# Optimization experiments

Hardware: AMD Instinct MI355X
Metric: run time of the kernel (lower is better)

The kernel has to match this reference:

```python
import jax, jax.numpy as jnp
import numpy as np

B, S, N_EMBD = 4, 4096, 1024
HIDDEN = 4 * N_EMBD
M_BITS_FC = 3
M_BITS_PROJ = 3
BLOCK_K = 32


def block_quant(v, m_bits, bk):
    """Block-floating-point quantization along the last (K) dim.
    Each block of `bk` elements shares an exponent derived from its max-abs;
    mantissas are rounded to `m_bits` bits. Straight-through estimator for grads."""
    *lead, K = v.shape
    vb = v.reshape(*lead, K // bk, bk)
    amax = jnp.max(jnp.abs(vb), axis=-1, keepdims=True)
    tiny = jnp.asarray(2.0 ** -126, v.dtype)
    e = jnp.floor(jnp.log2(jnp.maximum(amax, tiny)))  # shared block exponent
    scale = jnp.exp2(e - m_bits)                       # quantization step
    q = jnp.round(vb / scale) * scale
    q = vb + jax.lax.stop_gradient(q - vb)             # STE
    return q.reshape(v.shape)


def lowprec_linear(x, w, b, m_bits, bk):
    # w: [out, in]; quantize both operands along the contraction dim.
    xq = block_quant(x, m_bits, bk)
    wq = block_quant(w, m_bits, bk)
    return jnp.einsum('bsk,nk->bsn', xq, wq) + b


def setup_inputs() -> dict:
    key = jax.random.key(0)
    k0, k1, k2 = jax.random.split(key, 3)
    x = jax.random.normal(k0, (B, S, N_EMBD), jnp.float32)
    w_fc = jax.random.normal(k1, (HIDDEN, N_EMBD), jnp.float32) * (1.0 / np.sqrt(N_EMBD))
    b_fc = jnp.zeros((HIDDEN,), jnp.float32)
    w_proj = jax.random.normal(k2, (N_EMBD, HIDDEN), jnp.float32) * (1.0 / np.sqrt(HIDDEN))
    b_proj = jnp.zeros((N_EMBD,), jnp.float32)
    return {"x": x, "w_fc": w_fc, "b_fc": b_fc, "w_proj": w_proj, "b_proj": b_proj}


def reference(x, w_fc, b_fc, w_proj, b_proj):
    h = lowprec_linear(x, w_fc, b_fc, M_BITS_FC, BLOCK_K)
    h = jax.nn.gelu(h, approximate=False)  # nn.GELU default = exact erf
    return lowprec_linear(h, w_proj, b_proj, M_BITS_PROJ, BLOCK_K)
```

## Files before the change

kernel.cpp:

```cpp
#include <hip/hip_runtime.h>
#include <hip/hip_bf16.h>

using bf16 = __hip_bfloat16;
typedef __attribute__((ext_vector_type(8))) short short8;
typedef __attribute__((ext_vector_type(4))) float f32x4;

#define DI __device__ __forceinline__

constexpr int MROWS = 16384;
constexpr int EMB   = 1024;
constexpr int HID   = 4096;

DI void gload16(const bf16* g, bf16* l) {
  __builtin_amdgcn_global_load_lds((const __attribute__((address_space(1))) void*)g,
                                   (__attribute__((address_space(3))) void*)l,
                                   16, 0, 0);
}

DI void qparams(float amax, float& scale, float& inv) {
  int eb = (int)((__float_as_uint(amax) >> 23) & 255u);
  eb = eb < 4 ? 4 : eb;
  scale = __uint_as_float((unsigned)(eb - 3) << 23);
  inv   = __uint_as_float((unsigned)(257 - eb) << 23);
}

__global__ void quant32(const float* __restrict__ in, bf16* __restrict__ out, int nblk) {
  int b = blockIdx.x * blockDim.x + threadIdx.x;
  if (b >= nblk) return;
  const f32x4* p = (const f32x4*)(in + (size_t)b * 32);
  f32x4 v[8];
  float amax = 0.f;
#pragma unroll
  for (int i = 0; i < 8; i++) {
    v[i] = p[i];
    amax = fmaxf(amax, fmaxf(fmaxf(fabsf(v[i][0]), fabsf(v[i][1])),
                             fmaxf(fabsf(v[i][2]), fabsf(v[i][3]))));
  }
  float scale, inv;
  qparams(amax, scale, inv);
  alignas(16) unsigned short us[32];
#pragma unroll
  for (int i = 0; i < 8; i++)
#pragma unroll
    for (int j = 0; j < 4; j++)
      us[i * 4 + j] = (unsigned short)(__float_as_uint(rintf(v[i][j] * inv) * scale) >> 16);
  short8* o = (short8*)(out + (size_t)b * 32);
#pragma unroll
  for (int i = 0; i < 4; i++) o[i] = *(short8*)(us + i * 8);
}

#define MFMA16(a, b, c) __builtin_amdgcn_mfma_f32_16x16x32_bf16(a, b, c, 0, 0, 0)
#define SBAR()    __builtin_amdgcn_s_barrier()
#define WAITVM(n) asm volatile("s_waitcnt vmcnt(" #n ")" ::: "memory")

#define DPPMAX(x, ctrl) \
  x = fmaxf(x, __int_as_float(__builtin_amdgcn_update_dpp( \
          0, __float_as_int(x), ctrl, 0xf, 0xf, false)));
DI float redmax16(float x) {
  DPPMAX(x, 0xB1) DPPMAX(x, 0x4E) DPPMAX(x, 0x124) DPPMAX(x, 0x128)
  return x;
}

#define Q_MFMA(MB, NB, BG) \
  __builtin_amdgcn_s_setprio(1); \
  _Pragma("unroll") for (int kk = 0; kk < 2; kk++) \
  _Pragma("unroll") for (int mi = 0; mi < 4; mi++) \
  _Pragma("unroll") for (int ni = 0; ni < 2; ni++) \
    acc[(MB) + mi][(NB) + ni] = MFMA16(af[mi * 2 + kk], BG[ni * 2 + kk], acc[(MB) + mi][(NB) + ni]); \
  __builtin_amdgcn_s_setprio(0);

#define RD_AF(mh) \
  _Pragma("unroll") for (int mi = 0; mi < 4; mi++) { \
    af[mi * 2]     = ldA(db, mh, mi, 0); \
    af[mi * 2 + 1] = ldA(db, mh, mi, 1); }

#define RD_B(half, dst) \
  _Pragma("unroll") for (int ni = 0; ni < 2; ni++) { \
    dst[ni * 2]     = ldB(db, half, ni, 0); \
    dst[ni * 2 + 1] = ldB(db, half, ni, 1); }

template<int Kd, int Nd, bool GQ>
__global__ void __launch_bounds__(512, 2)
gemm8(const bf16* __restrict__ Ap, const bf16* __restrict__ Bp,
      const float* __restrict__ bias, void* __restrict__ Cout) {
  __shared__ alignas(16) bf16 SH[65536];
  bf16* Abuf = SH;
  bf16* Bbuf = SH + 32768;

  const int tid  = threadIdx.x;
  const int lane = tid & 63, wave = tid >> 6;
  const int l16  = lane & 15, lhi = lane >> 4;
  const int wr   = wave >> 2, wc  = wave & 3;

  const int idx  = blockIdx.x >> 3;
  const int xid  = blockIdx.x & 7;
  const int brow = (xid * 8 + (idx & 7)) * 256;
  const int bcol = (idx >> 3) * 256;

  const int r0 = tid >> 3;
  const int sl = (tid & 7) ^ (r0 & 7);
  const bf16* asrc = Ap + (size_t)(brow + r0) * Kd + sl * 8;
  const bf16* bsrc = Bp + (size_t)(bcol + r0) * Kd + sl * 8;

  auto stA = [&](int tt, int half) {
    const bf16* s = asrc + (size_t)half * 128 * Kd + tt * 64;
    bf16* d = Abuf + ((tt & 1) * 2 + half) * 8192 + tid * 8;
    gload16(s, d); gload16(s + (size_t)64 * Kd, d + 4096);
  };
  auto stB = [&](int tt, int half) {
    const bf16* s = bsrc + (size_t)half * 128 * Kd + tt * 64;
    bf16* d = Bbuf + ((tt & 1) * 2 + half) * 8192 + tid * 8;
    gload16(s, d); gload16(s + (size_t)64 * Kd, d + 4096);
  };

  const int sx = l16 & 7;
  const int arow = wr * 16 + l16;
  auto ldA = [&](int db, int mh, int mi, int kk) -> short8 {
    return *(const short8*)(Abuf + (db * 2 + mh) * 8192 +
                            (mi * 32 + arow) * 64 + ((kk * 4 + lhi) ^ sx) * 8);
  };
  const int brl = wc * 32 + l16;
  auto ldB = [&](int db, int half, int ni, int kk) -> short8 {
    return *(const short8*)(Bbuf + (db * 2 + half) * 8192 +
                            (brl + ni * 16) * 64 + ((kk * 4 + lhi) ^ sx) * 8);
  };

  f32x4 acc[8][4] = {};
  short8 af[8], bgl[4], bgh[4];

  constexpr int NT = Kd / 64;

  stA(0, 0); stB(0, 0); stB(0, 1); stA(0, 1);
  stA(1, 0); stB(1, 0); stB(1, 1);
  WAITVM(6); SBAR();

  for (int t = 0; t <= NT - 3; ++t) {
    const int db = t & 1;
    RD_AF(0) RD_B(0, bgl) RD_B(1, bgh)
    stA(t + 1, 1);
    Q_MFMA(0, 0, bgl)
    stA(t + 2, 0);
    Q_MFMA(0, 2, bgh)
    stB(t + 2, 0);
    RD_AF(1)
    stB(t + 2, 1);
    Q_MFMA(4, 0, bgl)
    Q_MFMA(4, 2, bgh)
    WAITVM(6); SBAR();
  }

  {
    const int db = (NT - 2) & 1;
    RD_AF(0) RD_B(0, bgl) RD_B(1, bgh)
    stA(NT - 1, 1);
    Q_MFMA(0, 0, bgl)
    Q_MFMA(0, 2, bgh)
    RD_AF(1)
    Q_MFMA(4, 0, bgl)
    Q_MFMA(4, 2, bgh)
    WAITVM(0); SBAR();
  }

  {
    const int db = (NT - 1) & 1;
    RD_AF(0) RD_B(0, bgl) RD_B(1, bgh)
    Q_MFMA(0, 0, bgl)
    Q_MFMA(0, 2, bgh)
    RD_AF(1)
    Q_MFMA(4, 0, bgl)
    Q_MFMA(4, 2, bgh)
  }

  const int cb = bcol + wc * 32;
  float bv[4];
#pragma unroll
  for (int n = 0; n < 4; n++) bv[n] = bias[cb + (n >> 1) * 128 + (n & 1) * 16 + l16];

  if constexpr (GQ) {
    bf16* outp = (bf16*)Cout;
#pragma unroll
    for (int mh2 = 0; mh2 < 2; mh2++) {
      __syncthreads();
#pragma unroll
      for (int mm = 0; mm < 4; mm++) {
        const int m = mh2 * 4 + mm;
        const int rl0 = mm * 32 + wr * 16 + lhi * 4;
#pragma unroll
        for (int r = 0; r < 4; r++) {
          float g[4];
#pragma unroll
          for (int n = 0; n < 4; n++) {
            float v = acc[m][n][r] + bv[n];
            g[n] = 0.5f * v * (1.0f + erff(v * 0.70710678118654752f));
          }
          const int rowb = (rl0 + r) * 256;
#pragma unroll
          for (int p = 0; p < 2; p++) {
            float am = redmax16(fmaxf(fabsf(g[p * 2]), fabsf(g[p * 2 + 1])));
            float sc, iv; qparams(am, sc, iv);
            const int c0 = wc * 32 + p * 128;
            SH[rowb + ((c0 + l16)      ^ (lhi << 4))] = __float2bfloat16(rintf(g[p * 2]     * iv) * sc);
            SH[rowb + ((c0 + 16 + l16) ^ (lhi << 4))] = __float2bfloat16(rintf(g[p * 2 + 1] * iv) * sc);
          }
        }
      }
      __syncthreads();
#pragma unroll
      for (int i = 0; i < 8; i++) {
        const int c   = i * 512 + tid;
        const int row = c >> 5, cc = c & 31;
        const int scc = cc ^ (((row >> 2) & 3) << 1);
        *(short8*)(outp + (size_t)(brow + mh2 * 128 + row) * Nd + bcol + cc * 8) =
            *(const short8*)(SH + (size_t)row * 256 + scc * 8);
      }
    }
  } else {
    float* outp = (float*)Cout;
#pragma unroll
    for (int m = 0; m < 8; m++) {
      const size_t rbase = (size_t)(brow + m * 32 + wr * 16 + lhi * 4);
#pragma unroll
      for (int r = 0; r < 4; r++) {
        const size_t ro = (rbase + r) * Nd;
#pragma unroll
        for (int n = 0; n < 4; n++)
          __builtin_nontemporal_store(acc[m][n][r] + bv[n],
              &outp[ro + cb + (n >> 1) * 128 + (n & 1) * 16 + l16]);
      }
    }
  }
}

extern "C" void kernel_launch(void* const* d_in, const int* in_sizes, int n_in,
                              void* d_out, int out_size, void* d_ws, size_t ws_size,
                              hipStream_t stream) {
  const float* x      = (const float*)d_in[0];
  const float* w_fc   = (const float*)d_in[1];
  const float* b_fc   = (const float*)d_in[2];
  const float* w_proj = (const float*)d_in[3];
  const float* b_proj = (const float*)d_in[4];

  char* ws = (char*)d_ws;
  bf16* xq  = (bf16*)ws;  ws += (size_t)MROWS * EMB * 2;
  bf16* wfq = (bf16*)ws;  ws += (size_t)HID * EMB * 2;
  bf16* wpq = (bf16*)ws;  ws += (size_t)EMB * HID * 2;
  bf16* hq  = (bf16*)ws;

  quant32<<<(MROWS * EMB / 32 + 255) / 256, 256, 0, stream>>>(x, xq, MROWS * EMB / 32);
  quant32<<<(HID * EMB / 32 + 255) / 256, 256, 0, stream>>>(w_fc, wfq, HID * EMB / 32);
  quant32<<<(EMB * HID / 32 + 255) / 256, 256, 0, stream>>>(w_proj, wpq, EMB * HID / 32);

  gemm8<EMB, HID, true ><<<(MROWS / 256) * (HID / 256), 512, 0, stream>>>(xq, wfq, b_fc, hq);
  gemm8<HID, EMB, false><<<(MROWS / 256) * (EMB / 256), 512, 0, stream>>>(hq, wpq, b_proj, (float*)d_out);
}
```

Before: 335.4 us.

## Give each FC GEMM block two output tiles and overlap next prefetch with epilogue

The first GEMM now launches 512 blocks, each computing two 256x256 tiles separated by 8192 rows. The prologue loads for the second tile are issued before the last MFMA stage and GELU epilogue of the first tile, which hides the pipeline fill. The epilogue also drops its LDS staging with two syncthreads and writes bf16 results straight to global memory with non-temporal scalar stores. This trades coalesced 16-byte stores for fewer barriers and frees LDS for the overlapped prefetch, at the cost of narrower, less coalesced writes.

```diff
diff --git a/kernel.cpp b/kernel.cpp
--- a/kernel.cpp
+++ b/kernel.cpp
@@ -79,7 +79,7 @@
     dst[ni * 2]     = ldB(db, half, ni, 0); \
     dst[ni * 2 + 1] = ldB(db, half, ni, 1); }
 
-template<int Kd, int Nd, bool GQ>
+template<int Kd, int Nd, bool GQ, int OT>
 __global__ void __launch_bounds__(512, 2)
 gemm8(const bf16* __restrict__ Ap, const bf16* __restrict__ Bp,
       const float* __restrict__ bias, void* __restrict__ Cout) {
@@ -92,10 +92,10 @@
   const int l16  = lane & 15, lhi = lane >> 4;
   const int wr   = wave >> 2, wc  = wave & 3;
 
-  const int idx  = blockIdx.x >> 3;
-  const int xid  = blockIdx.x & 7;
-  const int brow = (xid * 8 + (idx & 7)) * 256;
-  const int bcol = (idx >> 3) * 256;
+  int brow, bcol;
+  const int idx = blockIdx.x >> 3, xid = blockIdx.x & 7;
+  if constexpr (OT == 2) { brow = (xid * 4 + (idx & 3)) * 256; bcol = (idx >> 2) * 256; }
+  else                   { brow = (xid * 8 + (idx & 7)) * 256; bcol = (idx >> 3) * 256; }
 
   const int r0 = tid >> 3;
   const int sl = (tid & 7) ^ (r0 & 7);
@@ -130,11 +130,39 @@
 
   constexpr int NT = Kd / 64;
 
-  stA(0, 0); stB(0, 0); stB(0, 1); stA(0, 1);
-  stA(1, 0); stB(1, 0); stB(1, 1);
-  WAITVM(6); SBAR();
-
-  for (int t = 0; t <= NT - 3; ++t) {
+  const int cb = bcol + wc * 32;
+  float bv[4];
+#pragma unroll
+  for (int n = 0; n < 4; n++) bv[n] = bias[cb + (n >> 1) * 128 + (n & 1) * 16 + l16];
+
+  auto epiGQ = [&](int browseg) {
+    unsigned short* outp = (unsigned short*)Cout;
+#pragma unroll
+    for (int m = 0; m < 8; m++) {
+#pragma unroll
+      for (int r = 0; r < 4; r++) {
+        float g[4];
+#pragma unroll
+        for (int n = 0; n < 4; n++) {
+          float v = acc[m][n][r] + bv[n];
+          g[n] = 0.5f * v * (1.0f + erff(v * 0.70710678118654752f));
+        }
+        const size_t ro = (size_t)(browseg + m * 32 + wr * 16 + lhi * 4 + r) * Nd;
+#pragma unroll
+        for (int p = 0; p < 2; p++) {
+          float am = redmax16(fmaxf(fabsf(g[p * 2]), fabsf(g[p * 2 + 1])));
+          float sc, iv; qparams(am, sc, iv);
+          unsigned short* o = outp + ro + cb + p * 128 + l16;
+          __builtin_nontemporal_store(
+              (unsigned short)(__float_as_uint(rintf(g[p * 2] * iv) * sc) >> 16), o);
+          __builtin_nontemporal_store(
+              (unsigned short)(__float_as_uint(rintf(g[p * 2 + 1] * iv) * sc) >> 16), o + 16);
+        }
+      }
+    }
+  };
+
+  auto main_iter = [&](int t) {
     const int db = t & 1;
     RD_AF(0) RD_B(0, bgl) RD_B(1, bgh)
     stA(t + 1, 1);
@@ -147,7 +175,13 @@
     Q_MFMA(4, 0, bgl)
     Q_MFMA(4, 2, bgh)
     WAITVM(6); SBAR();
-  }
+  };
+
+  stA(0, 0); stB(0, 0); stB(0, 1); stA(0, 1);
+  stA(1, 0); stB(1, 0); stB(1, 1);
+  WAITVM(6); SBAR();
+
+  for (int t = 0; t <= NT - 3; ++t) main_iter(t);
 
   {
     const int db = (NT - 2) & 1;
@@ -161,71 +195,74 @@
     WAITVM(0); SBAR();
   }
 
-  {
-    const int db = (NT - 1) & 1;
-    RD_AF(0) RD_B(0, bgl) RD_B(1, bgh)
-    Q_MFMA(0, 0, bgl)
-    Q_MFMA(0, 2, bgh)
-    RD_AF(1)
-    Q_MFMA(4, 0, bgl)
-    Q_MFMA(4, 2, bgh)
-  }
-
-  const int cb = bcol + wc * 32;
-  float bv[4];
-#pragma unroll
-  for (int n = 0; n < 4; n++) bv[n] = bias[cb + (n >> 1) * 128 + (n & 1) * 16 + l16];
-
-  if constexpr (GQ) {
-    bf16* outp = (bf16*)Cout;
-#pragma unroll
-    for (int mh2 = 0; mh2 < 2; mh2++) {
-      __syncthreads();
-#pragma unroll
-      for (int mm = 0; mm < 4; mm++) {
-        const int m = mh2 * 4 + mm;
-        const int rl0 = mm * 32 + wr * 16 + lhi * 4;
+  if constexpr (OT == 2) {
+    asrc += (size_t)8192 * Kd;
+    {
+      const int db = (NT - 1) & 1;
+      stA(0, 0); stB(0, 0); stB(0, 1); stA(0, 1);
+      RD_AF(0) RD_B(0, bgl) RD_B(1, bgh)
+      Q_MFMA(0, 0, bgl)
+      Q_MFMA(0, 2, bgh)
+      RD_AF(1)
+      Q_MFMA(4, 0, bgl)
+      Q_MFMA(4, 2, bgh)
+      SBAR();
+    }
+    epiGQ(brow);
+    stA(1, 0); stB(1, 0); stB(1, 1);
+    WAITVM(6); SBAR();
+#pragma unroll
+    for (int m = 0; m < 8; m++)
+#pragma unroll
+      for (int n = 0; n < 4; n++) acc[m][n] = f32x4{0.f, 0.f, 0.f, 0.f};
+
+    for (int t = 0; t <= NT - 3; ++t) main_iter(t);
+    {
+      const int db = (NT - 2) & 1;
+      RD_AF(0) RD_B(0, bgl) RD_B(1, bgh)
+      stA(NT - 1, 1);
+      Q_MFMA(0, 0, bgl)
+      Q_MFMA(0, 2, bgh)
+      RD_AF(1)
+      Q_MFMA(4, 0, bgl)
+      Q_MFMA(4, 2, bgh)
+      WAITVM(0); SBAR();
+    }
+    {
+      const int db = (NT - 1) & 1;
+      RD_AF(0) RD_B(0, bgl) RD_B(1, bgh)
+      Q_MFMA(0, 0, bgl)
+      Q_MFMA(0, 2, bgh)
+      RD_AF(1)
+      Q_MFMA(4, 0, bgl)
+      Q_MFMA(4, 2, bgh)
+    }
+    epiGQ(brow + 8192);
+  } else {
+    {
+      const int db = (NT - 1) & 1;
+      RD_AF(0) RD_B(0, bgl) RD_B(1, bgh)
+      Q_MFMA(0, 0, bgl)
+      Q_MFMA(0, 2, bgh)
+      RD_AF(1)
+      Q_MFMA(4, 0, bgl)
+      Q_MFMA(4, 2, bgh)
+    }
+    if constexpr (GQ) {
+      epiGQ(brow);
+    } else {
+      float* outp = (float*)Cout;
+#pragma unroll
+      for (int m = 0; m < 8; m++) {
+        const size_t rbase = (size_t)(brow + m * 32 + wr * 16 + lhi * 4);
 #pragma unroll
         for (int r = 0; r < 4; r++) {
-          float g[4];
-#pragma unroll
-          for (int n = 0; n < 4; n++) {
-            float v = acc[m][n][r] + bv[n];
-            g[n] = 0.5f * v * (1.0f + erff(v * 0.70710678118654752f));
-          }
-          const int rowb = (rl0 + r) * 256;
-#pragma unroll
-          for (int p = 0; p < 2; p++) {
-            float am = redmax16(fmaxf(fabsf(g[p * 2]), fabsf(g[p * 2 + 1])));
-            float sc, iv; qparams(am, sc, iv);
-            const int c0 = wc * 32 + p * 128;
-            SH[rowb + ((c0 + l16)      ^ (lhi << 4))] = __float2bfloat16(rintf(g[p * 2]     * iv) * sc);
-            SH[rowb + ((c0 + 16 + l16) ^ (lhi << 4))] = __float2bfloat16(rintf(g[p * 2 + 1] * iv) * sc);
-          }
+          const size_t ro = (rbase + r) * Nd;
+#pragma unroll
+          for (int n = 0; n < 4; n++)
+            __builtin_nontemporal_store(acc[m][n][r] + bv[n],
+                &outp[ro + cb + (n >> 1) * 128 + (n & 1) * 16 + l16]);
         }
-      }
-      __syncthreads();
-#pragma unroll
-      for (int i = 0; i < 8; i++) {
-        const int c   = i * 512 + tid;
-        const int row = c >> 5, cc = c & 31;
-        const int scc = cc ^ (((row >> 2) & 3) << 1);
-        *(short8*)(outp + (size_t)(brow + mh2 * 128 + row) * Nd + bcol + cc * 8) =
-            *(const short8*)(SH + (size_t)row * 256 + scc * 8);
-      }
-    }
-  } else {
-    float* outp = (float*)Cout;
-#pragma unroll
-    for (int m = 0; m < 8; m++) {
-      const size_t rbase = (size_t)(brow + m * 32 + wr * 16 + lhi * 4);
-#pragma unroll
-      for (int r = 0; r < 4; r++) {
-        const size_t ro = (rbase + r) * Nd;
-#pragma unroll
-        for (int n = 0; n < 4; n++)
-          __builtin_nontemporal_store(acc[m][n][r] + bv[n],
-              &outp[ro + cb + (n >> 1) * 128 + (n & 1) * 16 + l16]);
       }
     }
   }
@@ -250,6 +287,6 @@
   quant32<<<(HID * EMB / 32 + 255) / 256, 256, 0, stream>>>(w_fc, wfq, HID * EMB / 32);
   quant32<<<(EMB * HID / 32 + 255) / 256, 256, 0, stream>>>(w_proj, wpq, EMB * HID / 32);
 
-  gemm8<EMB, HID, true ><<<(MROWS / 256) * (HID / 256), 512, 0, stream>>>(xq, wfq, b_fc, hq);
-  gemm8<HID, EMB, false><<<(MROWS / 256) * (EMB / 256), 512, 0, stream>>>(hq, wpq, b_proj, (float*)d_out);
-}
+  gemm8<EMB, HID, true,  2><<<512, 512, 0, stream>>>(xq, wfq, b_fc, hq);
+  gemm8<HID, EMB, false, 1><<<(MROWS / 256) * (EMB / 256), 512, 0, stream>>>(hq, wpq, b_proj, (float*)d_out);
+}
```

Result: no change. 331.7 us (-1.1%).

## Use MX-FP8 scaled MFMA with per-block exponents instead of bf16 GEMMs

Applied to the files above, without the earlier changes.

Quantizes activations and weights to FP8 E4M3 mantissas plus a separate per-32-element exponent array, then runs both GEMMs with the scaled 16x16x128 f8f6f4 MFMA. This halves operand bytes and uses the faster FP8 matrix path. The GELU epilogue now writes FP8 codes and scales directly. A runtime probe kernel detects the scale/operand layout convention and selects among kernel variants, with a bf16 fallback. Extra no-op launches and the probe add fixed launch overhead.

```diff
diff --git a/kernel.cpp b/kernel.cpp
--- a/kernel.cpp
+++ b/kernel.cpp
@@ -1,9 +1,15 @@
 #include <hip/hip_runtime.h>
 #include <hip/hip_bf16.h>
+#include <cstdint>
 
 using bf16 = __hip_bfloat16;
 typedef __attribute__((ext_vector_type(8))) short short8;
 typedef __attribute__((ext_vector_type(4))) float f32x4;
+typedef __attribute__((ext_vector_type(4))) unsigned u32x4;
+typedef __attribute__((ext_vector_type(2))) unsigned u32x2;
+typedef __attribute__((ext_vector_type(8))) int i32x8;
+typedef __attribute__((ext_vector_type(4))) int i32x4;
+typedef __attribute__((ext_vector_type(2))) int i32x2;
 
 #define DI __device__ __forceinline__
 
@@ -11,45 +17,11 @@
 constexpr int EMB   = 1024;
 constexpr int HID   = 4096;
 
-DI void gload16(const bf16* g, bf16* l) {
+DI void gload16(const void* g, void* l) {
   __builtin_amdgcn_global_load_lds((const __attribute__((address_space(1))) void*)g,
-                                   (__attribute__((address_space(3))) void*)l,
-                                   16, 0, 0);
-}
-
-DI void qparams(float amax, float& scale, float& inv) {
-  int eb = (int)((__float_as_uint(amax) >> 23) & 255u);
-  eb = eb < 4 ? 4 : eb;
-  scale = __uint_as_float((unsigned)(eb - 3) << 23);
-  inv   = __uint_as_float((unsigned)(257 - eb) << 23);
-}
-
-__global__ void quant32(const float* __restrict__ in, bf16* __restrict__ out, int nblk) {
-  int b = blockIdx.x * blockDim.x + threadIdx.x;
-  if (b >= nblk) return;
-  const f32x4* p = (const f32x4*)(in + (size_t)b * 32);
-  f32x4 v[8];
-  float amax = 0.f;
-#pragma unroll
-  for (int i = 0; i < 8; i++) {
-    v[i] = p[i];
-    amax = fmaxf(amax, fmaxf(fmaxf(fabsf(v[i][0]), fabsf(v[i][1])),
-                             fmaxf(fabsf(v[i][2]), fabsf(v[i][3]))));
-  }
-  float scale, inv;
-  qparams(amax, scale, inv);
-  alignas(16) unsigned short us[32];
-#pragma unroll
-  for (int i = 0; i < 8; i++)
-#pragma unroll
-    for (int j = 0; j < 4; j++)
-      us[i * 4 + j] = (unsigned short)(__float_as_uint(rintf(v[i][j] * inv) * scale) >> 16);
-  short8* o = (short8*)(out + (size_t)b * 32);
-#pragma unroll
-  for (int i = 0; i < 4; i++) o[i] = *(short8*)(us + i * 8);
-}
-
-#define MFMA16(a, b, c) __builtin_amdgcn_mfma_f32_16x16x32_bf16(a, b, c, 0, 0, 0)
+                                   (__attribute__((address_space(3))) void*)l, 16, 0, 0);
+}
+
 #define SBAR()    __builtin_amdgcn_s_barrier()
 #define WAITVM(n) asm volatile("s_waitcnt vmcnt(" #n ")" ::: "memory")
 
@@ -61,28 +33,313 @@
   return x;
 }
 
-#define Q_MFMA(MB, NB, BG) \
+DI uint8_t enc8(float n) {
+  unsigned b = __float_as_uint(n);
+  unsigned s = (b >> 24) & 0x80u;
+  unsigned e = (b >> 23) & 0xffu;
+  return (uint8_t)(e ? (s | ((e - 123u) << 3) | ((b >> 20) & 7u)) : s);
+}
+
+__global__ void mxprobe(int* flag) {
+  i32x8 a, b;
+#pragma unroll
+  for (int i = 0; i < 8; i++) { a[i] = (i < 2) ? 0x38383838 : 0; b[i] = 0x38383838; }
+  f32x4 c = {0.f, 0.f, 0.f, 0.f};
+  const int l16 = threadIdx.x & 15, lhi = (threadIdx.x & 63) >> 4;
+  int s0 = (l16 == 5 && lhi == 0) ? (int)0x80808080 : 0x7f7f7f7f;
+  int s1 = 0x7f7f7f7f;
+  f32x4 d = __builtin_amdgcn_mfma_scale_f32_16x16x128_f8f6f4(a, b, c, 0, 0, 0, s0, 0, s1);
+  float x00 = __shfl(d[0], 0, 64);
+  float x50 = __shfl(d[1], 16, 64);
+  float x05 = __shfl(d[0], 5, 64);
+  if (threadIdx.x == 0) {
+    int f = 4;
+    if (x00 == 32.f) {
+      if      (x50 == 40.f && x05 == 32.f) f = 0;
+      else if (x50 == 64.f && x05 == 32.f) f = 1;
+      else if (x05 == 40.f && x50 == 32.f) f = 2;
+      else if (x05 == 64.f && x50 == 32.f) f = 3;
+    }
+    flag[0] = f;
+  }
+}
+
+template<int BPRL, bool APACK>
+__global__ void quant8(const float* __restrict__ in, uint8_t* __restrict__ out,
+                       uint8_t* __restrict__ sT, int nblk, int nr,
+                       const int* __restrict__ mxfl) {
+  if (mxfl[0] > 3) return;
+  int b = blockIdx.x * blockDim.x + threadIdx.x;
+  if (b >= nblk) return;
+  const f32x4* p = (const f32x4*)(in + (size_t)b * 32);
+  f32x4 v[8]; float amax = 0.f;
+#pragma unroll
+  for (int i = 0; i < 8; i++) {
+    v[i] = p[i];
+    amax = fmaxf(amax, fmaxf(fmaxf(fabsf(v[i][0]), fabsf(v[i][1])),
+                             fmaxf(fabsf(v[i][2]), fabsf(v[i][3]))));
+  }
+  int eb = (int)((__float_as_uint(amax) >> 23) & 255u); eb = eb < 4 ? 4 : eb;
+  float inv = __uint_as_float((unsigned)(257 - eb) << 23);
+  u32x4 d0, d1;
+#pragma unroll
+  for (int i = 0; i < 8; i++) {
+    unsigned w = 0;
+#pragma unroll
+    for (int j = 0; j < 4; j++) w |= (unsigned)enc8(rintf(v[i][j] * inv)) << (j * 8);
+    if (i < 4) d0[i] = w; else d1[i - 4] = w;
+  }
+  *(u32x4*)(out + (size_t)b * 32) = d0;
+  *(u32x4*)(out + (size_t)b * 32 + 16) = d1;
+  int row = b >> BPRL, blk = b & ((1 << BPRL) - 1);
+  size_t si = APACK ? (size_t)((blk << 5) + (row & 31)) * (nr >> 5) + (row >> 5)
+                    : (size_t)((blk << 4) + (row & 15)) * (nr >> 4) + (row >> 4);
+  sT[si] = (uint8_t)eb;
+}
+
+__global__ void quant32(const float* __restrict__ in, bf16* __restrict__ out, int nblk,
+                        const int* __restrict__ mxfl) {
+  if (mxfl[0] <= 3) return;
+  int b = blockIdx.x * blockDim.x + threadIdx.x;
+  if (b >= nblk) return;
+  const f32x4* p = (const f32x4*)(in + (size_t)b * 32);
+  f32x4 v[8]; float amax = 0.f;
+#pragma unroll
+  for (int i = 0; i < 8; i++) {
+    v[i] = p[i];
+    amax = fmaxf(amax, fmaxf(fmaxf(fabsf(v[i][0]), fabsf(v[i][1])),
+                             fmaxf(fabsf(v[i][2]), fabsf(v[i][3]))));
+  }
+  int eb = (int)((__float_as_uint(amax) >> 23) & 255u); eb = eb < 4 ? 4 : eb;
+  float scale = __uint_as_float((unsigned)(eb - 3) << 23);
+  float inv   = __uint_as_float((unsigned)(257 - eb) << 23);
+  alignas(16) unsigned short us[32];
+#pragma unroll
+  for (int i = 0; i < 8; i++)
+#pragma unroll
+    for (int j = 0; j < 4; j++)
+      us[i * 4 + j] = (unsigned short)(__float_as_uint(rintf(v[i][j] * inv) * scale) >> 16);
+  short8* o = (short8*)(out + (size_t)b * 32);
+#pragma unroll
+  for (int i = 0; i < 4; i++) o[i] = *(short8*)(us + i * 8);
+}
+
+#define QUAD(MH, NH, BG, SAD, SBW) { \
+  _Pragma("unroll") for (int mp = 0; mp < 2; mp++) { \
+    i32x8 a0 = ldA(db, MH, mp * 2); \
+    i32x8 a1 = ldA(db, MH, mp * 2 + 1); \
+    __builtin_amdgcn_s_setprio(1); \
+    _Pragma("unroll") for (int ni = 0; ni < 2; ni++) { \
+      int sb = (int)(((unsigned)((SBW) >> (ni * 8)) & 0xffu) * 0x01010101u); \
+      int s0 = (int)(((unsigned)((SAD) >> (mp * 16)) & 0xffu) * 0x01010101u); \
+      int s1 = (int)(((unsigned)((SAD) >> (mp * 16 + 8)) & 0xffu) * 0x01010101u); \
+      int p0 = fl ? sb : s0, q0 = fl ? s0 : sb; \
+      int p1 = fl ? sb : s1, q1 = fl ? s1 : sb; \
+      acc[(MH)*4+mp*2][(NH)*2+ni] = __builtin_amdgcn_mfma_scale_f32_16x16x128_f8f6f4( \
+          a0, BG[ni], acc[(MH)*4+mp*2][(NH)*2+ni], 0, 0, 0, p0, 0, q0); \
+      acc[(MH)*4+mp*2+1][(NH)*2+ni] = __builtin_amdgcn_mfma_scale_f32_16x16x128_f8f6f4( \
+          a1, BG[ni], acc[(MH)*4+mp*2+1][(NH)*2+ni], 0, 0, 0, p1, 0, q1); \
+    } \
+    __builtin_amdgcn_s_setprio(0); \
+  } }
+
+template<int Kd, int Nd, bool GQ, int LAY>
+__global__ void __launch_bounds__(512, 2)
+mxgemm(const uint8_t* __restrict__ Ap, const uint8_t* __restrict__ Bp,
+       const uint8_t* __restrict__ sA, const uint8_t* __restrict__ sB,
+       const float* __restrict__ bias, void* __restrict__ Cout,
+       uint8_t* __restrict__ sOut, const int* __restrict__ mxfl) {
+  const int f = mxfl[0];
+  if (f > 3 || (f & 1) != LAY) return;
+  const int fl = (f >> 1) & 1;
+
+  __shared__ alignas(16) uint8_t SH[131072];
+  uint8_t* Abuf = SH;
+  uint8_t* Bbuf = SH + 65536;
+
+  const int tid = threadIdx.x;
+  const int lane = tid & 63, wave = tid >> 6;
+  const int l16 = lane & 15, lhi = lane >> 4;
+  const int wr = wave >> 2, wc = wave & 3;
+
+  const int idx = blockIdx.x >> 3, xid = blockIdx.x & 7;
+  const int brow = (xid * 8 + (idx & 7)) * 256;
+  const int bcol = (idx >> 3) * 256;
+
+  const int r0 = tid >> 3;
+  const int sl = (tid & 7) ^ (r0 & 7);
+  const uint8_t* asrc = Ap + (size_t)(brow + r0) * Kd + sl * 16;
+  const uint8_t* bsrc = Bp + (size_t)(bcol + r0) * Kd + sl * 16;
+
+  auto stA = [&](int tt, int half) {
+    const uint8_t* s = asrc + (size_t)half * 128 * Kd + tt * 128;
+    uint8_t* d = Abuf + ((tt & 1) * 2 + half) * 16384 + tid * 16;
+    gload16(s, d); gload16(s + (size_t)64 * Kd, d + 8192);
+  };
+  auto stB = [&](int tt, int half) {
+    const uint8_t* s = bsrc + (size_t)half * 128 * Kd + tt * 128;
+    uint8_t* d = Bbuf + ((tt & 1) * 2 + half) * 16384 + tid * 16;
+    gload16(s, d); gload16(s + (size_t)64 * Kd, d + 8192);
+  };
+
+  const int sx = l16 & 7;
+  auto ld8 = [&](const uint8_t* base) -> i32x8 {
+    i32x8 r;
+    if constexpr (LAY == 0) {
+      i32x4 lo = *(const i32x4*)(base + (((lhi * 2 + 0) ^ sx) << 4));
+      i32x4 hi = *(const i32x4*)(base + (((lhi * 2 + 1) ^ sx) << 4));
+      r[0] = lo[0]; r[1] = lo[1]; r[2] = lo[2]; r[3] = lo[3];
+      r[4] = hi[0]; r[5] = hi[1]; r[6] = hi[2]; r[7] = hi[3];
+    } else {
+#pragma unroll
+      for (int s = 0; s < 4; s++) {
+        i32x2 q = *(const i32x2*)(base + ((((s * 2 + (lhi >> 1)) ^ sx) << 4) + (lhi & 1) * 8));
+        r[2 * s] = q[0]; r[2 * s + 1] = q[1];
+      }
+    }
+    return r;
+  };
+  auto ldA = [&](int db, int mh, int mt) -> i32x8 {
+    return ld8(Abuf + (db * 2 + mh) * 16384 + (mt * 32 + wr * 16 + l16) * 128);
+  };
+  auto ldB = [&](int db, int nh, int ni) -> i32x8 {
+    return ld8(Bbuf + (db * 2 + nh) * 16384 + (wc * 32 + ni * 16 + l16) * 128);
+  };
+
+  u32x2 curA, nxA; unsigned curB0, curB1, nxB0, nxB1;
+  auto gA = [&](int t) -> u32x2 {
+    return *(const u32x2*)(sA + ((size_t)(4 * t + lhi) * 32 + wr * 16 + l16) * (MROWS >> 5)
+                              + (brow >> 5));
+  };
+  auto gB = [&](int t, unsigned& b0, unsigned& b1) {
+    const uint8_t* p = sB + ((size_t)(4 * t + lhi) * 16 + l16) * (Nd >> 4) + (bcol >> 4) + wc * 2;
+    b0 = *(const unsigned short*)p;
+    b1 = *(const unsigned short*)(p + 8);
+  };
+
+  f32x4 acc[8][4] = {};
+  i32x8 bgl[2], bgh[2];
+
+  constexpr int NT = Kd / 128;
+
+  stA(0, 0); stB(0, 0); stB(0, 1); stA(0, 1);
+  curA = gA(0); gB(0, curB0, curB1);
+  stA(1, 0); stB(1, 0); stB(1, 1);
+  WAITVM(6); SBAR();
+
+  for (int t = 0; t <= NT - 3; ++t) {
+    const int db = t & 1;
+    bgl[0] = ldB(db, 0, 0); bgl[1] = ldB(db, 0, 1);
+    bgh[0] = ldB(db, 1, 0); bgh[1] = ldB(db, 1, 1);
+    nxA = gA(t + 1); gB(t + 1, nxB0, nxB1);
+    stA(t + 1, 1);
+    QUAD(0, 0, bgl, curA[0], curB0)
+    QUAD(0, 1, bgh, curA[0], curB1)
+    stA(t + 2, 0);
+    QUAD(1, 0, bgl, curA[1], curB0)
+    stB(t + 2, 0); stB(t + 2, 1);
+    QUAD(1, 1, bgh, curA[1], curB1)
+    WAITVM(6); SBAR();
+    curA = nxA; curB0 = nxB0; curB1 = nxB1;
+  }
+
+  {
+    const int db = (NT - 2) & 1;
+    bgl[0] = ldB(db, 0, 0); bgl[1] = ldB(db, 0, 1);
+    bgh[0] = ldB(db, 1, 0); bgh[1] = ldB(db, 1, 1);
+    nxA = gA(NT - 1); gB(NT - 1, nxB0, nxB1);
+    stA(NT - 1, 1);
+    QUAD(0, 0, bgl, curA[0], curB0)
+    QUAD(0, 1, bgh, curA[0], curB1)
+    QUAD(1, 0, bgl, curA[1], curB0)
+    QUAD(1, 1, bgh, curA[1], curB1)
+    WAITVM(0); SBAR();
+    curA = nxA; curB0 = nxB0; curB1 = nxB1;
+  }
+
+  {
+    const int db = (NT - 1) & 1;
+    bgl[0] = ldB(db, 0, 0); bgl[1] = ldB(db, 0, 1);
+    bgh[0] = ldB(db, 1, 0); bgh[1] = ldB(db, 1, 1);
+    QUAD(0, 0, bgl, curA[0], curB0)
+    QUAD(0, 1, bgh, curA[0], curB1)
+    QUAD(1, 0, bgl, curA[1], curB0)
+    QUAD(1, 1, bgh, curA[1], curB1)
+  }
+
+  const int cb = bcol + wc * 32;
+  float bv[4];
+#pragma unroll
+  for (int n = 0; n < 4; n++) bv[n] = bias[cb + (n >> 1) * 128 + (n & 1) * 16 + l16];
+
+  if constexpr (GQ) {
+    uint8_t* hq = (uint8_t*)Cout;
+#pragma unroll
+    for (int m = 0; m < 8; m++) {
+#pragma unroll
+      for (int r = 0; r < 4; r++) {
+        float g[4];
+#pragma unroll
+        for (int n = 0; n < 4; n++) {
+          float v = acc[m][n][r] + bv[n];
+          g[n] = 0.5f * v * (1.0f + erff(v * 0.70710678118654752f));
+        }
+        const int row = brow + m * 32 + wr * 16 + lhi * 4 + r;
+        const size_t ro = (size_t)row * Nd;
+#pragma unroll
+        for (int p = 0; p < 2; p++) {
+          float am = redmax16(fmaxf(fabsf(g[p * 2]), fabsf(g[p * 2 + 1])));
+          int eb = (int)((__float_as_uint(am) >> 23) & 255u); eb = eb < 4 ? 4 : eb;
+          float iv = __uint_as_float((unsigned)(257 - eb) << 23);
+          hq[ro + cb + p * 128 + l16]      = enc8(rintf(g[p * 2] * iv));
+          hq[ro + cb + p * 128 + 16 + l16] = enc8(rintf(g[p * 2 + 1] * iv));
+          if (l16 == 0) {
+            const int blk = (cb >> 5) + p * 4;
+            sOut[((size_t)((blk << 5) + (row & 31)) << 9) + (row >> 5)] = (uint8_t)eb;
+          }
+        }
+      }
+    }
+  } else {
+    float* outp = (float*)Cout;
+#pragma unroll
+    for (int m = 0; m < 8; m++) {
+      const size_t rbase = (size_t)(brow + m * 32 + wr * 16 + lhi * 4);
+#pragma unroll
+      for (int r = 0; r < 4; r++) {
+        const size_t ro = (rbase + r) * Nd;
+#pragma unroll
+        for (int n = 0; n < 4; n++)
+          __builtin_nontemporal_store(acc[m][n][r] + bv[n],
+              &outp[ro + cb + (n >> 1) * 128 + (n & 1) * 16 + l16]);
+      }
+    }
+  }
+}
+
+#define BMFMA(a, b, c) __builtin_amdgcn_mfma_f32_16x16x32_bf16(a, b, c, 0, 0, 0)
+#define BQ_MFMA(MB, NB, BG) \
   __builtin_amdgcn_s_setprio(1); \
   _Pragma("unroll") for (int kk = 0; kk < 2; kk++) \
   _Pragma("unroll") for (int mi = 0; mi < 4; mi++) \
   _Pragma("unroll") for (int ni = 0; ni < 2; ni++) \
-    acc[(MB) + mi][(NB) + ni] = MFMA16(af[mi * 2 + kk], BG[ni * 2 + kk], acc[(MB) + mi][(NB) + ni]); \
+    acc[(MB) + mi][(NB) + ni] = BMFMA(af[mi * 2 + kk], BG[ni * 2 + kk], acc[(MB) + mi][(NB) + ni]); \
   __builtin_amdgcn_s_setprio(0);
-
-#define RD_AF(mh) \
+#define BRD_AF(mh) \
   _Pragma("unroll") for (int mi = 0; mi < 4; mi++) { \
     af[mi * 2]     = ldA(db, mh, mi, 0); \
     af[mi * 2 + 1] = ldA(db, mh, mi, 1); }
-
-#define RD_B(half, dst) \
+#define BRD_B(half, dst) \
   _Pragma("unroll") for (int ni = 0; ni < 2; ni++) { \
     dst[ni * 2]     = ldB(db, half, ni, 0); \
     dst[ni * 2 + 1] = ldB(db, half, ni, 1); }
 
 template<int Kd, int Nd, bool GQ>
 __global__ void __launch_bounds__(512, 2)
-gemm8(const bf16* __restrict__ Ap, const bf16* __restrict__ Bp,
-      const float* __restrict__ bias, void* __restrict__ Cout) {
+bgemm(const bf16* __restrict__ Ap, const bf16* __restrict__ Bp,
+      const float* __restrict__ bias, void* __restrict__ Cout,
+      const int* __restrict__ mxfl) {
+  if (mxfl[0] <= 3) return;
   __shared__ alignas(16) bf16 SH[65536];
   bf16* Abuf = SH;
   bf16* Bbuf = SH + 32768;
@@ -127,7 +384,6 @@
 
   f32x4 acc[8][4] = {};
   short8 af[8], bgl[4], bgh[4];
-
   constexpr int NT = Kd / 64;
 
   stA(0, 0); stB(0, 0); stB(0, 1); stA(0, 1);
@@ -136,39 +392,37 @@
 
   for (int t = 0; t <= NT - 3; ++t) {
     const int db = t & 1;
-    RD_AF(0) RD_B(0, bgl) RD_B(1, bgh)
+    BRD_AF(0) BRD_B(0, bgl) BRD_B(1, bgh)
     stA(t + 1, 1);
-    Q_MFMA(0, 0, bgl)
+    BQ_MFMA(0, 0, bgl)
     stA(t + 2, 0);
-    Q_MFMA(0, 2, bgh)
+    BQ_MFMA(0, 2, bgh)
     stB(t + 2, 0);
-    RD_AF(1)
+    BRD_AF(1)
     stB(t + 2, 1);
-    Q_MFMA(4, 0, bgl)
-    Q_MFMA(4, 2, bgh)
+    BQ_MFMA(4, 0, bgl)
+    BQ_MFMA(4, 2, bgh)
     WAITVM(6); SBAR();
   }
-
   {
     const int db = (NT - 2) & 1;
-    RD_AF(0) RD_B(0, bgl) RD_B(1, bgh)
+    BRD_AF(0) BRD_B(0, bgl) BRD_B(1, bgh)
     stA(NT - 1, 1);
-    Q_MFMA(0, 0, bgl)
-    Q_MFMA(0, 2, bgh)
-    RD_AF(1)
-    Q_MFMA(4, 0, bgl)
-    Q_MFMA(4, 2, bgh)
+    BQ_MFMA(0, 0, bgl)
+    BQ_MFMA(0, 2, bgh)
+    BRD_AF(1)
+    BQ_MFMA(4, 0, bgl)
+    BQ_MFMA(4, 2, bgh)
     WAITVM(0); SBAR();
   }
-
   {
     const int db = (NT - 1) & 1;
-    RD_AF(0) RD_B(0, bgl) RD_B(1, bgh)
-    Q_MFMA(0, 0, bgl)
-    Q_MFMA(0, 2, bgh)
-    RD_AF(1)
-    Q_MFMA(4, 0, bgl)
-    Q_MFMA(4, 2, bgh)
+    BRD_AF(0) BRD_B(0, bgl) BRD_B(1, bgh)
+    BQ_MFMA(0, 0, bgl)
+    BQ_MFMA(0, 2, bgh)
+    BRD_AF(1)
+    BQ_MFMA(4, 0, bgl)
+    BQ_MFMA(4, 2, bgh)
   }
 
   const int cb = bcol + wc * 32;
@@ -197,7 +451,9 @@
 #pragma unroll
           for (int p = 0; p < 2; p++) {
             float am = redmax16(fmaxf(fabsf(g[p * 2]), fabsf(g[p * 2 + 1])));
-            float sc, iv; qparams(am, sc, iv);
+            int eb = (int)((__float_as_uint(am) >> 23) & 255u); eb = eb < 4 ? 4 : eb;
+            float sc = __uint_as_float((unsigned)(eb - 3) << 23);
+            float iv = __uint_as_float((unsigned)(257 - eb) << 23);
             const int c0 = wc * 32 + p * 128;
             SH[rowb + ((c0 + l16)      ^ (lhi << 4))] = __float2bfloat16(rintf(g[p * 2]     * iv) * sc);
             SH[rowb + ((c0 + 16 + l16) ^ (lhi << 4))] = __float2bfloat16(rintf(g[p * 2 + 1] * iv) * sc);
@@ -210,10 +466,11 @@
         const int c   = i * 512 + tid;
         const int row = c >> 5, cc = c & 31;
         const int scc = cc ^ (((row >> 2) & 3) << 1);
-        *(short8*)(outp + (size_t)(brow + mh2 * 128 + row) * Nd + bcol + cc * 8) =
+        *(short8*)((bf16*)Cout + (size_t)(brow + mh2 * 128 + row) * Nd + bcol + cc * 8) =
             *(const short8*)(SH + (size_t)row * 256 + scc * 8);
       }
     }
+    (void)outp;
   } else {
     float* outp = (float*)Cout;
 #pragma unroll
@@ -240,16 +497,44 @@
   const float* w_proj = (const float*)d_in[3];
   const float* b_proj = (const float*)d_in[4];
 
-  char* ws = (char*)d_ws;
-  bf16* xq  = (bf16*)ws;  ws += (size_t)MROWS * EMB * 2;
-  bf16* wfq = (bf16*)ws;  ws += (size_t)HID * EMB * 2;
-  bf16* wpq = (bf16*)ws;  ws += (size_t)EMB * HID * 2;
-  bf16* hq  = (bf16*)ws;
-
-  quant32<<<(MROWS * EMB / 32 + 255) / 256, 256, 0, stream>>>(x, xq, MROWS * EMB / 32);
-  quant32<<<(HID * EMB / 32 + 255) / 256, 256, 0, stream>>>(w_fc, wfq, HID * EMB / 32);
-  quant32<<<(EMB * HID / 32 + 255) / 256, 256, 0, stream>>>(w_proj, wpq, EMB * HID / 32);
-
-  gemm8<EMB, HID, true ><<<(MROWS / 256) * (HID / 256), 512, 0, stream>>>(xq, wfq, b_fc, hq);
-  gemm8<HID, EMB, false><<<(MROWS / 256) * (EMB / 256), 512, 0, stream>>>(hq, wpq, b_proj, (float*)d_out);
-}
+  char* base = (char*)d_ws;
+  const size_t MB = 1ull << 20;
+  int* mxfl = (int*)(base + ws_size - 4096);
+
+  uint8_t* xq8  = (uint8_t*)(base);
+  uint8_t* wfq8 = (uint8_t*)(base + 16 * MB);
+  uint8_t* wpq8 = (uint8_t*)(base + 20 * MB);
+  uint8_t* hq8  = (uint8_t*)(base + 24 * MB);
+  uint8_t* sxA  = (uint8_t*)(base + 88 * MB);
+  uint8_t* swfc = (uint8_t*)(base + 88 * MB + 512 * 1024);
+  uint8_t* swpj = (uint8_t*)(base + 88 * MB + 640 * 1024);
+  uint8_t* shA  = (uint8_t*)(base + 89 * MB);
+  bf16* xqb  = (bf16*)(base);
+  bf16* wfqb = (bf16*)(base + 32 * MB);
+  bf16* wpqb = (bf16*)(base + 40 * MB);
+  bf16* hqb  = (bf16*)(base + 48 * MB);
+  const bool dual = ws_size >= 177 * MB;
+
+  mxprobe<<<1, 64, 0, stream>>>(mxfl);
+
+  quant8<5, true ><<<2048, 256, 0, stream>>>(x,      xq8,  sxA,  MROWS * EMB / 32, MROWS, mxfl);
+  quant8<5, false><<< 512, 256, 0, stream>>>(w_fc,   wfq8, swfc, HID * EMB / 32,   HID,   mxfl);
+  quant8<7, false><<< 512, 256, 0, stream>>>(w_proj, wpq8, swpj, EMB * HID / 32,   EMB,   mxfl);
+  if (dual) {
+    quant32<<<2048, 256, 0, stream>>>(x,      xqb,  MROWS * EMB / 32, mxfl);
+    quant32<<< 512, 256, 0, stream>>>(w_fc,   wfqb, HID * EMB / 32,   mxfl);
+    quant32<<< 512, 256, 0, stream>>>(w_proj, wpqb, EMB * HID / 32,   mxfl);
+  }
+
+  const int g1 = (MROWS / 256) * (HID / 256);
+  const int g2 = (MROWS / 256) * (EMB / 256);
+  mxgemm<EMB, HID, true, 0><<<g1, 512, 0, stream>>>(xq8, wfq8, sxA, swfc, b_fc, hq8, shA, mxfl);
+  mxgemm<EMB, HID, true, 1><<<g1, 512, 0, stream>>>(xq8, wfq8, sxA, swfc, b_fc, hq8, shA, mxfl);
+  if (dual)
+    bgemm<EMB, HID, true ><<<g1, 512, 0, stream>>>(xqb, wfqb, b_fc, hqb, mxfl);
+
+  mxgemm<HID, EMB, false, 0><<<g2, 512, 0, stream>>>(hq8, wpq8, shA, swpj, b_proj, (float*)d_out, nullptr, mxfl);
+  mxgemm<HID, EMB, false, 1><<<g2, 512, 0, stream>>>(hq8, wpq8, shA, swpj, b_proj, (float*)d_out, nullptr, mxfl);
+  if (dual)
+    bgemm<HID, EMB, false><<<g2, 512, 0, stream>>>(hqb, wpqb, b_proj, (float*)d_out, mxfl);
+}
```

Result: slower. 354.8 us (+5.8%).
